# Kernel tuning notes

Hardware: AMD Instinct MI355X
Metric: run time of the kernel (lower is better)

The kernel has to match this reference:

```python
import jax, jax.numpy as jnp
import numpy as np

B, SQ, SKV = 4, 2048, 2048
IN_Q, IN_KV = 1024, 1024
H, D = 16, 64            # num_heads, hidden_channels (per-head dim)
OUT = 1024
ROPE_BASE = 4096.0


def _rope(x, base):
    # x: (..., items, D). Interleaved rotate-half RoPE over last dim.
    d = x.shape[-1]
    s = x.shape[-2]
    inv_freq = base ** (-jnp.arange(0, d, 2, dtype=x.dtype) / d)      # (D/2,)
    ang = jnp.arange(s, dtype=x.dtype)[:, None] * inv_freq[None, :]   # (S, D/2)
    cos = jnp.repeat(jnp.cos(ang), 2, axis=-1)                        # (S, D)
    sin = jnp.repeat(jnp.sin(ang), 2, axis=-1)
    xp = x.reshape(x.shape[:-1] + (d // 2, 2))
    x_rot = jnp.stack([-xp[..., 1], xp[..., 0]], axis=-1).reshape(x.shape)
    return x * cos + x_rot * sin


def setup_inputs() -> dict:
    key = jax.random.key(0)
    ks = jax.random.split(key, 8)
    sc = 0.02
    return {
        "q": jax.random.normal(ks[0], (B, SQ, IN_Q), jnp.float32),
        "kv": jax.random.normal(ks[1], (B, SKV, IN_KV), jnp.float32),
        # weights stored (in, out): y = x @ W + b  (equiv. to torch Linear)
        "Wq": jax.random.normal(ks[2], (IN_Q, H * D), jnp.float32) * sc,
        "bq": jnp.zeros((H * D,), jnp.float32),
        "Wkv": jax.random.normal(ks[3], (IN_KV, 2 * D), jnp.float32) * sc,
        "bkv": jnp.zeros((2 * D,), jnp.float32),
        "Wo": jax.random.normal(ks[4], (H * D, OUT), jnp.float32) * sc,
        "bo": jnp.zeros((OUT,), jnp.float32),
    }


def reference(q, kv, Wq, bq, Wkv, bkv, Wo, bo):
    # Q projection -> (B, H, SQ, D)
    qh = (q @ Wq + bq).reshape(B, SQ, H, D).transpose(0, 2, 1, 3)
    # KV projection (multi-query: single shared K/V head) -> (B, SKV, D) each
    kvp = kv @ Wkv + bkv
    k, v = kvp[..., :D], kvp[..., D:]
    # Rotary positional encoding on the item axis
    qh = _rope(qh, ROPE_BASE)
    k = _rope(k, ROPE_BASE)
    # Scaled dot-product attention with broadcast single-head K/V (MQA)
    scale = 1.0 / jnp.sqrt(jnp.asarray(D, qh.dtype))
    scores = jnp.einsum("bhqd,bkd->bhqk", qh, k) * scale   # (B,H,SQ,SKV)
    attn = jax.nn.softmax(scores, axis=-1)
    h = jnp.einsum("bhqk,bkd->bhqd", attn, v)              # (B,H,SQ,D)
    # Merge heads and output projection
    h = h.transpose(0, 2, 1, 3).reshape(B, SQ, H * D)
    return h @ Wo + bo
```

## Files before the change

### kernel.cpp

```cpp
#include <hip/hip_runtime.h>
#include <math.h>

typedef __bf16 bf16;
typedef __bf16 bf16x4 __attribute__((ext_vector_type(4)));
typedef __bf16 bf16x8 __attribute__((ext_vector_type(8)));
typedef float floatx4 __attribute__((ext_vector_type(4)));

#define MFMA16(a, b, c) __builtin_amdgcn_mfma_f32_16x16x32_bf16(a, b, c, 0, 0, 0)

#if __has_builtin(__builtin_amdgcn_exp2f)
#define EXP2F(x) __builtin_amdgcn_exp2f(x)
#else
#define EXP2F(x) exp2f(x)
#endif

constexpr int Bc = 4, SQc = 2048, SKVc = 2048, Hc = 16, Dc = 64;
#define QSCALE 0.18033688011112042f

__device__ __forceinline__ void glds16(const bf16* g, bf16* lds_base, int lane) {
#if __has_builtin(__builtin_amdgcn_global_load_lds)
  __builtin_amdgcn_global_load_lds(
      (const __attribute__((address_space(1))) void*)g,
      (__attribute__((address_space(3))) void*)lds_base, 16, 0, 0);
#else
  *(bf16x8*)(lds_base + 8 * lane) = *(const bf16x8*)g;
#endif
}

__global__ void cvt_bf16(const float* __restrict__ in, bf16* __restrict__ out) {
  const size_t i = ((size_t)blockIdx.x * 256 + threadIdx.x) * 4;
  const float4 v = *(const float4*)&in[i];
  bf16x4 o = {(bf16)v.x, (bf16)v.y, (bf16)v.z, (bf16)v.w};
  *(bf16x4*)&out[i] = o;
}

__global__ void rope_tab_build(float2* __restrict__ tab) {
  const int i = blockIdx.x * 256 + threadIdx.x;
  const int pos = i >> 5, f = i & 31;
  const float ang = (float)pos * exp2f(-0.375f * (float)f);
  float sn, cs;
  sincosf(ang, &sn, &cs);
  tab[i] = make_float2(cs, sn);
}

__global__ void transpose_cvt(const float* __restrict__ in, bf16* __restrict__ out,
                              int K, int N) {
  __shared__ bf16 T[64][72];
  const int tid = threadIdx.x;
  const int n0 = blockIdx.x * 64, k0 = blockIdx.y * 64;
  const int tr = tid >> 4, tc4 = (tid & 15) * 4;
#pragma unroll
  for (int i = 0; i < 4; i++) {
    const int k = tr + 16 * i;
    const float4 v = *(const float4*)&in[(size_t)(k0 + k) * N + n0 + tc4];
    T[tc4 + 0][k] = (bf16)v.x;
    T[tc4 + 1][k] = (bf16)v.y;
    T[tc4 + 2][k] = (bf16)v.z;
    T[tc4 + 3][k] = (bf16)v.w;
  }
  __syncthreads();
  const int nr = tid >> 2, kc = (tid & 3) * 8;
#pragma unroll
  for (int hf = 0; hf < 2; hf++)
    *(bf16x8*)&out[(size_t)(n0 + nr) * K + k0 + kc + 32 * hf] =
        *(const bf16x8*)&T[nr][kc + 32 * hf];
}

__device__ __forceinline__ void gemm_kloop(const bf16* __restrict__ A,
                                           const bf16* __restrict__ BT, int m0,
                                           int n0, int tid, int wave, int lane,
                                           int m, int g, bf16* As, bf16* Bs,
                                           floatx4 (*acc)[2], int mq, int nq) {
  const int r_ = tid >> 3, p_ = tid & 7;
  const bf16* pA[4];
  const bf16* pB[2];
#pragma unroll
  for (int q = 0; q < 4; q++) {
    const int r = r_ + q * 32;
    const int s = p_ ^ (r & 7);
    pA[q] = &A[(size_t)(m0 + r) * 1024 + 8 * s];
    if (q < 2) pB[q] = &BT[(size_t)(n0 + r) * 1024 + 8 * s];
  }

  for (int k0 = 0; k0 < 1024; k0 += 64) {
    __syncthreads();
#pragma unroll
    for (int q = 0; q < 4; q++)
      glds16(pA[q] + k0, &As[(q * 4 + wave) * 512], lane);
#pragma unroll
    for (int q = 0; q < 2; q++)
      glds16(pB[q] + k0, &Bs[(q * 4 + wave) * 512], lane);
    __syncthreads();

    bf16x8 bb[2][2];
#pragma unroll
    for (int j = 0; j < 2; j++) {
      const int row = nq + 16 * j + m;
#pragma unroll
      for (int kh = 0; kh < 2; kh++)
        bb[j][kh] = *(const bf16x8*)&Bs[row * 64 + 8 * ((g + 4 * kh) ^ (row & 7))];
    }
#pragma unroll
    for (int i = 0; i < 4; i++) {
      const int row = mq + 16 * i + m;
      const bf16x8 a0 = *(const bf16x8*)&As[row * 64 + 8 * (g ^ (row & 7))];
      const bf16x8 a1 = *(const bf16x8*)&As[row * 64 + 8 * ((g + 4) ^ (row & 7))];
#pragma unroll
      for (int j = 0; j < 2; j++) {
        acc[i][j] = MFMA16(a0, bb[j][0], acc[i][j]);
        acc[i][j] = MFMA16(a1, bb[j][1], acc[i][j]);
      }
    }
  }
}

__global__ __launch_bounds__(256, 4) void gemm_qkv(
    const bf16* __restrict__ qA, const bf16* __restrict__ qBT,
    const float* __restrict__ qb, const bf16* __restrict__ kvA,
    const bf16* __restrict__ kvBT, const float* __restrict__ kvb,
    const float2* __restrict__ tab, bf16* __restrict__ qh,
    bf16* __restrict__ kko, bf16* __restrict__ vto) {
  __shared__ bf16 As[128 * 64];
  __shared__ bf16 Bs[64 * 64];

  const int tid = threadIdx.x, lane = tid & 63, wave = tid >> 6;
  const int m = lane & 15, g = lane >> 4;
  const int m0 = blockIdx.x * 128;
  const bool isQ = (blockIdx.y < 16);
  const int n0 = isQ ? blockIdx.y * 64 : (blockIdx.y - 16) * 64;
  const bf16* A = isQ ? qA : kvA;
  const bf16* BT = isQ ? qBT : kvBT;
  const float* bias = isQ ? qb : kvb;
  const int mq = (wave >> 1) * 64, nq = (wave & 1) * 32;

  floatx4 z = {0.f, 0.f, 0.f, 0.f};
  floatx4 acc[4][2];
#pragma unroll
  for (int i = 0; i < 4; i++)
#pragma unroll
    for (int j = 0; j < 2; j++) acc[i][j] = z;

  gemm_kloop(A, BT, m0, n0, tid, wave, lane, m, g, As, Bs, acc, mq, nq);

  const int rq = 4 * g;
#pragma unroll
  for (int j = 0; j < 2; j++) {
    const int col = n0 + nq + 16 * j + m;
    const float bv = bias[col];
#pragma unroll
    for (int i = 0; i < 4; i++) {
#pragma unroll
      for (int r = 0; r < 4; r++) {
        const int row = m0 + mq + 16 * i + rq + r;
        float v = acc[i][j][r] + bv;
        const float vp = __shfl_xor(v, 1);
        if (isQ) {
          const int d = col & 63, hh = col >> 6;
          const int pos = row & (SQc - 1), b = row >> 11;
          const float2 cssn = tab[pos * 32 + (d >> 1)];
          const float res = (d & 1) ? (v * cssn.x + vp * cssn.y)
                                    : (v * cssn.x - vp * cssn.y);
          qh[(((size_t)(b * Hc + hh) * SQc) + pos) * Dc + d] = (bf16)(res * QSCALE);
        } else {
          const int pos = row & (SKVc - 1), b = row >> 11;
          const size_t fb = (size_t)b * (SKVc * Dc);
          if (col < 64) {
            const int d = col;
            const float2 cssn = tab[pos * 32 + (d >> 1)];
            const float res = (d & 1) ? (v * cssn.x + vp * cssn.y)
                                      : (v * cssn.x - vp * cssn.y);
            const int kc = (pos >> 4) * 2 + (d >> 5);
            const int kl = ((d >> 3) & 3) * 16 + (pos & 15);
            kko[fb + (size_t)kc * 512 + kl * 8 + (d & 7)] = (bf16)res;
          } else {
            const int d = col - 64;
            const int vc = (pos >> 6) * 8 + (d >> 4) * 2 + ((pos >> 5) & 1);
            const int vl = ((pos >> 3) & 3) * 16 + (d & 15);
            vto[fb + (size_t)vc * 512 + vl * 8 + (pos & 7)] = (bf16)v;
          }
        }
      }
    }
  }
}

__global__ __launch_bounds__(256, 4) void gemm_out(
    const bf16* __restrict__ A, const bf16* __restrict__ BT,
    const float* __restrict__ bias, float* __restrict__ out) {
  __shared__ bf16 As[128 * 64];
  __shared__ bf16 Bs[64 * 64];

  const int tid = threadIdx.x, lane = tid & 63, wave = tid >> 6;
  const int m = lane & 15, g = lane >> 4;
  const int m0 = blockIdx.x * 128, n0 = blockIdx.y * 64;
  const int mq = (wave >> 1) * 64, nq = (wave & 1) * 32;

  floatx4 z = {0.f, 0.f, 0.f, 0.f};
  floatx4 acc[4][2];
#pragma unroll
  for (int i = 0; i < 4; i++)
#pragma unroll
    for (int j = 0; j < 2; j++) acc[i][j] = z;

  gemm_kloop(A, BT, m0, n0, tid, wave, lane, m, g, As, Bs, acc, mq, nq);

  const int rq = 4 * g;
#pragma unroll
  for (int j = 0; j < 2; j++) {
    const int col = n0 + nq + 16 * j + m;
    const float bv = bias[col];
#pragma unroll
    for (int i = 0; i < 4; i++)
#pragma unroll
      for (int r = 0; r < 4; r++) {
        const int row = m0 + mq + 16 * i + rq + r;
        out[(size_t)row * 1024 + col] = acc[i][j][r] + bv;
      }
  }
}

__global__ __launch_bounds__(512, 4) void attn_v5(
    const bf16* __restrict__ qh, const bf16* __restrict__ kk,
    const bf16* __restrict__ vt, bf16* __restrict__ hout) {
  const int bid = blockIdx.x;
  const int qt = bid & 7, h = (bid >> 3) & 15, b = bid >> 7;
  const int tid = threadIdx.x, lane = tid & 63, wave = tid >> 6;
  const int m = lane & 15, g = lane >> 4;

  __shared__ bf16 Kb[2][4096];
  __shared__ bf16 Vb[4096];
  __shared__ bf16 Pb[8][2][16][68];

  const int q0 = qt * 256 + wave * 32;
  const bf16* qp = qh + (((size_t)(b * Hc + h) * SQc) + q0 + m) * Dc + 8 * g;
  bf16x8 bq[2][2];
#pragma unroll
  for (int s = 0; s < 2; s++) {
    bq[s][0] = *(const bf16x8*)(qp + (size_t)(16 * s) * Dc);
    bq[s][1] = *(const bf16x8*)(qp + (size_t)(16 * s) * Dc + 32);
  }

  const bf16 one = (bf16)1.0f;
  const bf16x8 ones = {one, one, one, one, one, one, one, one};

  floatx4 z = {0.f, 0.f, 0.f, 0.f};
  floatx4 accO[2][4];
  floatx4 lacc[2] = {z, z};
#pragma unroll
  for (int s = 0; s < 2; s++)
#pragma unroll
    for (int t = 0; t < 4; t++) accO[s][t] = z;

  const size_t fb = (size_t)b * (SKVc * Dc);
  const bf16* kg = kk + fb + 8 * lane;
  const bf16* vg = vt + fb + 8 * lane;

  glds16(kg + (size_t)wave * 512, &Kb[0][wave * 512], lane);
  __syncthreads();

  for (int it = 0; it < 32; ++it) {
    const int cur = it & 1;
    if (it) __syncthreads();
    glds16(vg + (size_t)(it * 8 + wave) * 512, &Vb[wave * 512], lane);
    if (it + 1 < 32)
      glds16(kg + (size_t)((it + 1) * 8 + wave) * 512, &Kb[cur ^ 1][wave * 512],
             lane);

    bf16x8 kfr[4][2];
#pragma unroll
    for (int c = 0; c < 4; c++) {
      kfr[c][0] = *(const bf16x8*)&Kb[cur][(2 * c + 0) * 512 + 8 * lane];
      kfr[c][1] = *(const bf16x8*)&Kb[cur][(2 * c + 1) * 512 + 8 * lane];
    }
#pragma unroll
    for (int s = 0; s < 2; s++) {
#pragma unroll
      for (int c = 0; c < 4; c++) {
        floatx4 sv = MFMA16(kfr[c][0], bq[s][0], z);
        sv = MFMA16(kfr[c][1], bq[s][1], sv);
        bf16x4 pk = {(bf16)EXP2F(sv[0]), (bf16)EXP2F(sv[1]), (bf16)EXP2F(sv[2]),
                     (bf16)EXP2F(sv[3])};
        *(bf16x4*)&Pb[wave][s][m][16 * c + 4 * g] = pk;
      }
    }
    __syncthreads();

    bf16x8 vf[4][2];
#pragma unroll
    for (int t = 0; t < 4; t++) {
      vf[t][0] = *(const bf16x8*)&Vb[(2 * t + 0) * 512 + 8 * lane];
      vf[t][1] = *(const bf16x8*)&Vb[(2 * t + 1) * 512 + 8 * lane];
    }
    __builtin_amdgcn_s_setprio(1);
#pragma unroll
    for (int s = 0; s < 2; s++) {
      const bf16x8 pa0 = *(const bf16x8*)&Pb[wave][s][m][8 * g];
      const bf16x8 pa1 = *(const bf16x8*)&Pb[wave][s][m][32 + 8 * g];
      lacc[s] = MFMA16(pa0, ones, lacc[s]);
      lacc[s] = MFMA16(pa1, ones, lacc[s]);
#pragma unroll
      for (int t = 0; t < 4; t++) {
        accO[s][t] = MFMA16(pa0, vf[t][0], accO[s][t]);
        accO[s][t] = MFMA16(pa1, vf[t][1], accO[s][t]);
      }
    }
    __builtin_amdgcn_s_setprio(0);
  }

#pragma unroll
  for (int s = 0; s < 2; s++) {
    floatx4 inv;
#pragma unroll
    for (int r = 0; r < 4; r++) inv[r] = 1.0f / lacc[s][r];
#pragma unroll
    for (int t = 0; t < 4; t++)
#pragma unroll
      for (int r = 0; r < 4; r++) {
        const int qrow = q0 + 16 * s + 4 * g + r;
        hout[((size_t)(b * SQc + qrow)) * (Hc * Dc) + h * Dc + 16 * t + m] =
            (bf16)(accO[s][t][r] * inv[r]);
      }
  }
}

extern "C" void kernel_launch(void* const* d_in, const int* in_sizes, int n_in,
                              void* d_out, int out_size, void* d_ws, size_t ws_size,
                              hipStream_t stream) {
  const float* q = (const float*)d_in[0];
  const float* kv = (const float*)d_in[1];
  const float* Wq = (const float*)d_in[2];
  const float* bq = (const float*)d_in[3];
  const float* Wkv = (const float*)d_in[4];
  const float* bkv = (const float*)d_in[5];
  const float* Wo = (const float*)d_in[6];
  const float* bo = (const float*)d_in[7];

  char* ws = (char*)d_ws;
  bf16* qbf = (bf16*)ws;
  bf16* kvbf = (bf16*)(ws + ((size_t)16 << 20));
  bf16* WqT = (bf16*)(ws + ((size_t)32 << 20));
  bf16* WkvT = (bf16*)(ws + ((size_t)34 << 20));
  float2* rtab = (float2*)(ws + ((size_t)34 << 20) + ((size_t)256 << 10));
  bf16* WoT = (bf16*)(ws + ((size_t)35 << 20));
  bf16* qh = (bf16*)(ws + ((size_t)37 << 20));
  bf16* kk = (bf16*)(ws + ((size_t)53 << 20));
  bf16* vt = (bf16*)(ws + ((size_t)54 << 20));
  bf16* hh = qbf;

  const int M = Bc * SQc;

  rope_tab_build<<<256, 256, 0, stream>>>(rtab);
  cvt_bf16<<<M, 256, 0, stream>>>(q, qbf);
  cvt_bf16<<<M, 256, 0, stream>>>(kv, kvbf);
  transpose_cvt<<<dim3(16, 16), 256, 0, stream>>>(Wq, WqT, 1024, 1024);
  transpose_cvt<<<dim3(2, 16), 256, 0, stream>>>(Wkv, WkvT, 1024, 128);
  transpose_cvt<<<dim3(16, 16), 256, 0, stream>>>(Wo, WoT, 1024, 1024);

  gemm_qkv<<<dim3(64, 18), 256, 0, stream>>>(qbf, WqT, bq, kvbf, WkvT, bkv, rtab,
                                             qh, kk, vt);
  attn_v5<<<Bc * Hc * (SQc / 256), 512, 0, stream>>>(qh, kk, vt, hh);
  gemm_out<<<dim3(64, 16), 256, 0, stream>>>(hh, WoT, bo, (float*)d_out);
}
```

Baseline: 258.0 us.

## Double-buffer LDS tiles in GEMM k-loop to overlap loads with MFMA

Converts the shared GEMM k-loop used by the QKV and output projection kernels to a two-stage LDS double buffer. The next k-tile is prefetched via global_load_lds, with a partial vmcnt wait before each compute phase, so memory latency can overlap with MFMA work. This is meant to hide the global-to-LDS latency that the old load, sync, compute sequence exposed. In exchange LDS use doubles and the launch bounds drop from 4 to 3 blocks per CU, which lowers occupancy.

```diff
diff --git a/kernel.cpp b/kernel.cpp
--- a/kernel.cpp
+++ b/kernel.cpp
@@ -69,7 +69,8 @@
 __device__ __forceinline__ void gemm_kloop(const bf16* __restrict__ A,
                                            const bf16* __restrict__ BT, int m0,
                                            int n0, int tid, int wave, int lane,
-                                           int m, int g, bf16* As, bf16* Bs,
+                                           int m, int g, bf16 (*As)[128 * 64],
+                                           bf16 (*Bs)[64 * 64],
                                            floatx4 (*acc)[2], int mq, int nq) {
   const int r_ = tid >> 3, p_ = tid & 7;
   const bf16* pA[4];
@@ -82,15 +83,28 @@
     if (q < 2) pB[q] = &BT[(size_t)(n0 + r) * 1024 + 8 * s];
   }
 
-  for (int k0 = 0; k0 < 1024; k0 += 64) {
-    __syncthreads();
-#pragma unroll
-    for (int q = 0; q < 4; q++)
-      glds16(pA[q] + k0, &As[(q * 4 + wave) * 512], lane);
-#pragma unroll
-    for (int q = 0; q < 2; q++)
-      glds16(pB[q] + k0, &Bs[(q * 4 + wave) * 512], lane);
-    __syncthreads();
+#pragma unroll
+  for (int q = 0; q < 4; q++) glds16(pA[q], &As[0][(q * 4 + wave) * 512], lane);
+#pragma unroll
+  for (int q = 0; q < 2; q++) glds16(pB[q], &Bs[0][(q * 4 + wave) * 512], lane);
+  __syncthreads();
+
+  for (int t = 0; t < 16; ++t) {
+    const int cur = t & 1;
+    if (t < 15) {
+      const int k0 = 64 * (t + 1);
+#pragma unroll
+      for (int q = 0; q < 4; q++)
+        glds16(pA[q] + k0, &As[cur ^ 1][(q * 4 + wave) * 512], lane);
+#pragma unroll
+      for (int q = 0; q < 2; q++)
+        glds16(pB[q] + k0, &Bs[cur ^ 1][(q * 4 + wave) * 512], lane);
+      asm volatile("s_waitcnt vmcnt(6)" ::: "memory");
+    } else {
+      asm volatile("s_waitcnt vmcnt(0)" ::: "memory");
+    }
+    __builtin_amdgcn_s_barrier();
+    __builtin_amdgcn_sched_barrier(0);
 
     bf16x8 bb[2][2];
 #pragma unroll
@@ -98,30 +112,34 @@
       const int row = nq + 16 * j + m;
 #pragma unroll
       for (int kh = 0; kh < 2; kh++)
-        bb[j][kh] = *(const bf16x8*)&Bs[row * 64 + 8 * ((g + 4 * kh) ^ (row & 7))];
+        bb[j][kh] =
+            *(const bf16x8*)&Bs[cur][row * 64 + 8 * ((g + 4 * kh) ^ (row & 7))];
     }
 #pragma unroll
     for (int i = 0; i < 4; i++) {
       const int row = mq + 16 * i + m;
-      const bf16x8 a0 = *(const bf16x8*)&As[row * 64 + 8 * (g ^ (row & 7))];
-      const bf16x8 a1 = *(const bf16x8*)&As[row * 64 + 8 * ((g + 4) ^ (row & 7))];
+      const bf16x8 a0 = *(const bf16x8*)&As[cur][row * 64 + 8 * (g ^ (row & 7))];
+      const bf16x8 a1 =
+          *(const bf16x8*)&As[cur][row * 64 + 8 * ((g + 4) ^ (row & 7))];
 #pragma unroll
       for (int j = 0; j < 2; j++) {
         acc[i][j] = MFMA16(a0, bb[j][0], acc[i][j]);
         acc[i][j] = MFMA16(a1, bb[j][1], acc[i][j]);
       }
     }
-  }
-}
-
-__global__ __launch_bounds__(256, 4) void gemm_qkv(
+    __builtin_amdgcn_sched_barrier(0);
+    __builtin_amdgcn_s_barrier();
+  }
+}
+
+__global__ __launch_bounds__(256, 3) void gemm_qkv(
     const bf16* __restrict__ qA, const bf16* __restrict__ qBT,
     const float* __restrict__ qb, const bf16* __restrict__ kvA,
     const bf16* __restrict__ kvBT, const float* __restrict__ kvb,
     const float2* __restrict__ tab, bf16* __restrict__ qh,
     bf16* __restrict__ kko, bf16* __restrict__ vto) {
-  __shared__ bf16 As[128 * 64];
-  __shared__ bf16 Bs[64 * 64];
+  __shared__ bf16 As[2][128 * 64];
+  __shared__ bf16 Bs[2][64 * 64];
 
   const int tid = threadIdx.x, lane = tid & 63, wave = tid >> 6;
   const int m = lane & 15, g = lane >> 4;
@@ -184,11 +202,11 @@
   }
 }
 
-__global__ __launch_bounds__(256, 4) void gemm_out(
+__global__ __launch_bounds__(256, 3) void gemm_out(
     const bf16* __restrict__ A, const bf16* __restrict__ BT,
     const float* __restrict__ bias, float* __restrict__ out) {
-  __shared__ bf16 As[128 * 64];
-  __shared__ bf16 Bs[64 * 64];
+  __shared__ bf16 As[2][128 * 64];
+  __shared__ bf16 Bs[2][64 * 64];
 
   const int tid = threadIdx.x, lane = tid & 63, wave = tid >> 6;
   const int m = lane & 15, g = lane >> 4;
```

Result: slower. 276.2 us (+7.0%).
